# Kernel tuning notes

Hardware: AMD Instinct MI355X
Metric: run time of the kernel (lower is better)

The kernel has to match this reference:

```python
import jax, jax.numpy as jnp
import numpy as np
from jax import lax

B, C_IN, H, W = 32, 96, 48, 48
D = C_IN          # d_inner = expand(1) * in_features
K, N, DT_RANK = 2, 16, 6   # k_group, d_state, ceil(D/16)


def setup_inputs() -> dict:
    key = jax.random.key(0)
    ks = jax.random.split(key, 10)
    s = 0.02
    return {
        "x": jax.random.normal(ks[0], (B, C_IN, H, W), jnp.float32),
        "in_proj_w": jax.random.normal(ks[1], (D, C_IN)) * s,
        "in_proj_b": jnp.zeros((D,)),
        "skip_w": jax.random.normal(ks[2], (1, 1, 5)) * s,
        "skip_b": jnp.zeros((1,)),
        "conv2d_w": jax.random.normal(ks[3], (D, 1, 3, 3)) * s,
        "conv2d_b": jnp.zeros((D,)),
        "local_w": jax.random.normal(ks[4], (D, 1, 3, 3)) * s,
        "local_b": jnp.zeros((D,)),
        "bn_gamma": jnp.ones((D,)),
        "bn_beta": jnp.zeros((D,)),
        "x_proj_w": jax.random.normal(ks[5], (K, DT_RANK + 2 * N, D)) * s,
        "dt_projs_w": jax.random.normal(ks[6], (K, D, DT_RANK)) * s,
        "dt_projs_b": jax.random.normal(ks[7], (K, D)) * s,
        "A_logs": jnp.tile(jnp.log(jnp.arange(1, N + 1, dtype=jnp.float32))[None], (K * D, 1)),
        "Ds": jnp.ones((K * D,)),
        "norm_gamma": jnp.ones((D,)),
        "norm_beta": jnp.zeros((D,)),
        "out_proj_w": jax.random.normal(ks[8], (C_IN, D)) * s,
        "out_proj_b": jnp.zeros((C_IN,)),
    }


def _dwconv2d(x, w, bias):
    # depthwise 3x3, NCHW
    y = lax.conv_general_dilated(x, w, (1, 1), "SAME", feature_group_count=x.shape[1],
                                 dimension_numbers=("NCHW", "OIHW", "NCHW"))
    return y + bias[None, :, None, None]


def _forward(x, in_proj_w, in_proj_b, skip_w, skip_b, conv2d_w, conv2d_b,
             local_w, local_b, bn_gamma, bn_beta, x_proj_w, dt_projs_w,
             dt_projs_b, A_logs, Ds, norm_gamma, norm_beta, out_proj_w, out_proj_b):
    b, c, h, w = x.shape
    L = h * w
    x_in = jnp.transpose(x, (0, 2, 3, 1))                       # [B,H,W,C]
    # skip gate: Conv1d(1,1,k=5) over channel axis of the spatial mean
    zm = jnp.mean(x_in, axis=(1, 2))[:, None, :]                # [B,1,C]
    z = lax.conv_general_dilated(zm, skip_w, (1,), "SAME",
                                 dimension_numbers=("NCH", "OIH", "NCH")) + skip_b[None, :, None]
    z = z[:, None]                                              # [B,1,1,C]
    x_feat = jnp.transpose(x_in @ in_proj_w.T + in_proj_b, (0, 3, 1, 2))  # [B,D,H,W]
    x_conv = jax.nn.silu(_dwconv2d(x_feat, conv2d_w, conv2d_b))
    # ---- dynamic center-similarity ordering (computed under no_grad) ----
    xc = lax.stop_gradient(x_conv)
    xf = xc.reshape(b, D, L)
    xn = xf / jnp.maximum(jnp.linalg.norm(xf, axis=1, keepdims=True), 1e-12)
    cf = xc[:, :, h // 2, w // 2]                               # [B,D]
    cn = cf / jnp.maximum(jnp.linalg.norm(cf, axis=1, keepdims=True), 1e-12)
    sim = jnp.einsum("bdl,bd->bl", xn, cn)
    sort_idx = jnp.argsort(-sim, axis=1)                        # descending similarity
    inv_idx = jnp.argsort(sort_idx, axis=1)
    # ---- DynamicCenterScan: sorted sequence and its reverse (k_group=2) ----
    xseq = jnp.take_along_axis(x_conv.reshape(b, D, L), sort_idx[:, None, :], axis=2)
    xs = jnp.stack([xseq, jnp.flip(xseq, -1)], axis=1)          # [B,K,D,L]
    # ---- SS2D selective-scan core ----
    x_dbl = jnp.einsum("bkdl,kcd->bkcl", xs, x_proj_w)
    dts, Bs, Cs = jnp.split(x_dbl, [DT_RANK, DT_RANK + N], axis=2)
    dts = jnp.einsum("bkrl,kdr->bkdl", dts, dt_projs_w)
    dts = jax.nn.softplus(dts + dt_projs_b[None, :, :, None])   # [B,K,D,L]
    A = -jnp.exp(A_logs.reshape(K, D, N))                       # [K,D,N]

    def step(hst, t):
        dt_l, B_l, C_l, x_l = t                                 # [B,K,D],[B,K,N],[B,K,N],[B,K,D]
        dA = jnp.exp(dt_l[..., None] * A)                       # [B,K,D,N]
        hst = dA * hst + (dt_l * x_l)[..., None] * B_l[:, :, None, :]
        y = jnp.einsum("bkdn,bkn->bkd", hst, C_l)
        return hst, y

    tmove = lambda a: jnp.moveaxis(a, -1, 0)
    h0 = jnp.zeros((b, K, D, N), x.dtype)
    _, ys_t = lax.scan(step, h0, (tmove(dts), tmove(Bs), tmove(Cs), tmove(xs)))
    ys = jnp.moveaxis(ys_t, 0, -1) + Ds.reshape(K, D)[None, :, :, None] * xs  # [B,K,D,L]
    # ---- DynamicCenterMerge: un-flip, sum directions, inverse permutation ----
    y = ys[:, 0] + jnp.flip(ys[:, 1], -1)
    y = jnp.take_along_axis(y, inv_idx[:, None, :], axis=2).reshape(b, D, h, w)
    # out_norm: LayerNorm over channels
    yl = jnp.transpose(y, (0, 2, 3, 1))
    mu = jnp.mean(yl, -1, keepdims=True)
    var = jnp.var(yl, -1, keepdims=True)
    yl = (yl - mu) / jnp.sqrt(var + 1e-5) * norm_gamma + norm_beta
    out_mamba = jnp.transpose(yl, (0, 3, 1, 2))
    # local path: depthwise conv + BatchNorm (batch stats, train mode) + SiLU
    lc = _dwconv2d(x_conv, local_w, local_b)
    bm = jnp.mean(lc, (0, 2, 3))
    bv = jnp.var(lc, (0, 2, 3))
    lc = (lc - bm[None, :, None, None]) * (bn_gamma / jnp.sqrt(bv + 1e-5))[None, :, None, None] + bn_beta[None, :, None, None]
    lc = jax.nn.silu(lc)
    out = out_mamba + lc
    # softmax over dim=1 of z (singleton) == all-ones gate; kept for faithfulness
    out = jnp.transpose(out, (0, 2, 3, 1)) * jax.nn.softmax(z, axis=1)
    out = out @ out_proj_w.T + out_proj_b
    return jnp.transpose(out, (0, 3, 1, 2))


def reference(x, in_proj_w, in_proj_b, skip_w, skip_b, conv2d_w, conv2d_b,
              local_w, local_b, bn_gamma, bn_beta, x_proj_w, dt_projs_w,
              dt_projs_b, A_logs, Ds, norm_gamma, norm_beta, out_proj_w, out_proj_b):
    return _forward(x, in_proj_w, in_proj_b, skip_w, skip_b, conv2d_w, conv2d_b,
                    local_w, local_b, bn_gamma, bn_beta, x_proj_w, dt_projs_w,
                    dt_projs_b, A_logs, Ds, norm_gamma, norm_beta, out_proj_w, out_proj_b)
```

## Files before the change

kernel.cpp:

```cpp
#include <hip/hip_runtime.h>
#include <hip/hip_bf16.h>


typedef __hip_bfloat16 bf16;
__device__ __forceinline__ float b2f(bf16 v) { return __bfloat162float(v); }
__device__ __forceinline__ float ldu(const void* p, int i, bool f32) {
  if (f32) return ((const float*)p)[i];
  return b2f(((const bf16*)p)[i]);
}
__device__ __forceinline__ float rcp_f(float x) { return __builtin_amdgcn_rcpf(x); }

#define LL 2304
#define NSEG 72

#define W_INT  0
#define B_IN   9216
#define W_C2D  9312
#define B_C2D  10176
#define W_LOC  10272
#define B_LOC  11136
#define BN_G   11232
#define BN_B   11328
#define W_XPT  11424
#define W_DT   19104
#define B_DT   20256
#define A2OF   20448
#define DSOF   23520
#define LN_G   23712
#define LN_B   23808
#define W_OUTT 23904
#define B_OUT  33120
#define WBUF_N 33280ul

#define O_WBUF  0ul
#define O_XFEAT 33280ul
#define O_XCONV 7111168ul
#define O_SIM   14189056ul
#define O_SIDX  14262784ul
#define O_XST   14336512ul
#define O_XSTD  21414400ul
#define O_RBUF  28492288ul
#define O_BC    29671936ul
#define O_DSUM  34390528ul
#define O_YMLM  34832896ul
#define O_STATS 41910784ul
#define O_AFLG  41910976ul
#define O_SCSH  41911040ul
#define O_FLAG  41911232ul
#define O_END   41911296ul

__global__ void k_detect(const void* x, float* flag) {
  int i = threadIdx.x;
  bool bad = false;
  const bf16* xb = (const bf16*)x;
#pragma unroll
  for (int r = 0; r < 4; ++r) {
    float v = b2f(xb[r * 64 + i]);
    if (!(fabsf(v) <= 1e4f)) bad = true;
  }
  bool any = __any(bad);
  if (i == 0) flag[0] = any ? 1.f : 0.f;
}

__global__ void k_prep(const void* ipw, const void* ipb, const void* c2w, const void* c2b,
                       const void* lw, const void* lb, const void* bng, const void* bnb,
                       const void* xpw, const void* dtw, const void* dtb, const void* alog,
                       const void* dss, const void* ng, const void* nb, const void* opw,
                       const void* opb, float* wb, const float* flag, float* aflag) {
  bool f = flag[0] > 0.5f;
  int i = blockIdx.x * 256 + threadIdx.x;
  if (i < 9216) {
    int r = i / 96, c = i % 96;
    wb[W_INT + c * 96 + r] = ldu(ipw, i, f);
    wb[W_OUTT + c * 96 + r] = ldu(opw, i, f);
  }
  if (i < 96) {
    wb[B_IN + i] = ldu(ipb, i, f); wb[B_C2D + i] = ldu(c2b, i, f); wb[B_LOC + i] = ldu(lb, i, f);
    wb[BN_G + i] = ldu(bng, i, f); wb[BN_B + i] = ldu(bnb, i, f); wb[LN_G + i] = ldu(ng, i, f);
    wb[LN_B + i] = ldu(nb, i, f); wb[B_OUT + i] = ldu(opb, i, f);
  }
  if (i < 864) { wb[W_C2D + i] = ldu(c2w, i, f); wb[W_LOC + i] = ldu(lw, i, f); }
  if (i < 7296) {
    int k = i / 3648, c = (i / 96) % 38, d = i % 96;
    wb[W_XPT + d * 80 + k * 38 + c] = ldu(xpw, i, f);
  }
  if (i < 1152) wb[W_DT + i] = ldu(dtw, i, f);
  if (i < 192) { wb[B_DT + i] = ldu(dtb, i, f); wb[DSOF + i] = ldu(dss, i, f); }
  if (i < 3072) {
    float av = expf(ldu(alog, i, f));
    wb[A2OF + i] = -av * 1.4426950408889634f;
    int n = i % 16;
    if (fabsf(av - (float)(n + 1)) > 1e-3f * (n + 1)) atomicAdd(aflag, 1.f);
  }
}

__global__ __launch_bounds__(128, 4)
void k_inproj(const void* __restrict__ x, const float* __restrict__ wb,
              float* __restrict__ xfeat, const float* __restrict__ flag) {
  int b = blockIdx.x / 36;
  int rest = blockIdx.x % 36;
  int half = rest / 18;
  int l = (rest % 18) * 128 + threadIdx.x;
  float acc[48];
#pragma unroll
  for (int j = 0; j < 48; ++j) acc[j] = wb[B_IN + half * 48 + j];
  bool f = flag[0] > 0.5f;
  if (f) {
    const float* xf = (const float*)x;
#pragma unroll 2
    for (int c = 0; c < 96; ++c) {
      float xc = xf[(b * 96 + c) * LL + l];
      const float* wr = wb + W_INT + c * 96 + half * 48;
#pragma unroll
      for (int j = 0; j < 48; ++j) acc[j] += xc * wr[j];
    }
  } else {
    const bf16* xb = (const bf16*)x;
#pragma unroll 2
    for (int c = 0; c < 96; ++c) {
      float xc = b2f(xb[(b * 96 + c) * LL + l]);
      const float* wr = wb + W_INT + c * 96 + half * 48;
#pragma unroll
      for (int j = 0; j < 48; ++j) acc[j] += xc * wr[j];
    }
  }
#pragma unroll
  for (int j = 0; j < 48; ++j) xfeat[(b * 96 + half * 48 + j) * LL + l] = acc[j];
}

__global__ __launch_bounds__(256, 8)
void k_conv_silu(const float* __restrict__ xfeat, const float* __restrict__ wb,
                 float* __restrict__ xconv) {
  int t = blockIdx.x * 256 + threadIdx.x;
  int l = t % LL; int d = (t / LL) % 96; int b = t / (LL * 96);
  int h = l / 48, w = l % 48;
  const float* wr = wb + W_C2D + d * 9;
  const float* src = xfeat + (b * 96 + d) * LL;
  float acc = wb[B_C2D + d];
#pragma unroll
  for (int ki = 0; ki < 3; ++ki) {
    int hh = h + ki - 1; if (hh < 0 || hh >= 48) continue;
#pragma unroll
    for (int kj = 0; kj < 3; ++kj) {
      int ww = w + kj - 1; if (ww < 0 || ww >= 48) continue;
      acc += src[hh * 48 + ww] * wr[ki * 3 + kj];
    }
  }
  xconv[t] = acc / (1.f + expf(-acc));
}

__global__ __launch_bounds__(256, 8)
void k_sim(const float* __restrict__ xconv, float* __restrict__ sim) {
  int b = blockIdx.x / 9;
  int l = (blockIdx.x % 9) * 256 + threadIdx.x;
  const float* base = xconv + (size_t)b * 96 * LL;
  float dot = 0, nrm = 0, cn = 0;
  for (int d = 0; d < 96; ++d) {
    float v = base[d * LL + l];
    float c = base[d * LL + 1176];
    dot += v * c; nrm += v * v; cn += c * c;
  }
  float den = fmaxf(sqrtf(nrm), 1e-12f) * fmaxf(sqrtf(cn), 1e-12f);
  sim[b * LL + l] = dot / den;
}

__global__ void k_sort(const float* __restrict__ sim, int* __restrict__ sidx) {
  __shared__ unsigned long long key[4096];
  int b = blockIdx.x;
  for (int i = threadIdx.x; i < 4096; i += 1024) {
    unsigned long long kv = ~0ull;
    if (i < LL) {
      unsigned u = __float_as_uint(sim[b * LL + i]);
      u = (u >> 31) ? ~u : (u | 0x80000000u);
      kv = (((unsigned long long)(~u)) << 32) | (unsigned)i;
    }
    key[i] = kv;
  }
  __syncthreads();
  for (int k = 2; k <= 4096; k <<= 1)
    for (int j = k >> 1; j > 0; j >>= 1) {
      for (int i = threadIdx.x; i < 4096; i += 1024) {
        int ij = i ^ j;
        if (ij > i) {
          unsigned long long a = key[i], c = key[ij];
          bool up = ((i & k) == 0);
          if ((a > c) == up) { key[i] = c; key[ij] = a; }
        }
      }
      __syncthreads();
    }
  for (int i = threadIdx.x; i < LL; i += 1024) sidx[b * LL + i] = (int)(key[i] & 0xffffffffu);
}

__global__ __launch_bounds__(256, 8)
void k_gatherd(const float* __restrict__ xconv, const int* __restrict__ sidx,
               float* __restrict__ xstd) {
  int t = blockIdx.x * 256 + threadIdx.x;
  int l = t % LL; int d = (t / LL) % 96; int b = t / (LL * 96);
  int p = sidx[b * LL + l];
  xstd[t] = xconv[((size_t)b * 96 + d) * LL + p];
}

__global__ __launch_bounds__(256, 4)
void k_tr_dl(const float* __restrict__ in, float* __restrict__ out) {
  __shared__ float tile[64 * 97];
  int b = blockIdx.x / 36;
  int l0 = (blockIdx.x % 36) * 64;
#pragma unroll
  for (int it = 0; it < 24; ++it) {
    int idx = it * 256 + threadIdx.x;
    int d = idx / 64, j = idx % 64;
    tile[j * 97 + d] = in[((size_t)b * 96 + d) * LL + l0 + j];
  }
  __syncthreads();
#pragma unroll
  for (int it = 0; it < 24; ++it) {
    int idx = it * 256 + threadIdx.x;
    int r = idx / 96, c = idx % 96;
    out[((size_t)b * LL + l0 + r) * 96 + c] = tile[r * 97 + c];
  }
}

__global__ __launch_bounds__(256, 4)
void k_tr_ld(const float* __restrict__ in, float* __restrict__ out) {
  __shared__ float tile[64 * 97];
  int b = blockIdx.x / 36;
  int l0 = (blockIdx.x % 36) * 64;
#pragma unroll
  for (int it = 0; it < 24; ++it) {
    int idx = it * 256 + threadIdx.x;
    int r = idx / 96, c = idx % 96;
    tile[r * 97 + c] = in[((size_t)b * LL + l0 + r) * 96 + c];
  }
  __syncthreads();
#pragma unroll
  for (int it = 0; it < 24; ++it) {
    int idx = it * 256 + threadIdx.x;
    int d = idx / 64, j = idx % 64;
    out[((size_t)b * 96 + d) * LL + l0 + j] = tile[j * 97 + d];
  }
}

template <int KSEL>
__global__ __launch_bounds__(128, 4)
void k_xdbl(const float* __restrict__ xstd, const float* __restrict__ wb,
            float* __restrict__ rbuf, float* __restrict__ bc) {
  int b = blockIdx.x / 18;
  int l = (blockIdx.x % 18) * 128 + threadIdx.x;
  float acc[38];
#pragma unroll
  for (int j = 0; j < 38; ++j) acc[j] = 0.f;
#pragma unroll 2
  for (int c = 0; c < 96; ++c) {
    float xc = xstd[((size_t)b * 96 + c) * LL + l];
    const float* wr = wb + W_XPT + c * 80 + KSEL * 38;
#pragma unroll
    for (int j = 0; j < 38; ++j) acc[j] += xc * wr[j];
  }
  int lout = KSEL ? (LL - 1 - l) : l;
  float4* r4 = (float4*)(rbuf + ((size_t)(b * 2 + KSEL) * LL + lout) * 8);
  r4[0] = make_float4(acc[0], acc[1], acc[2], acc[3]);
  r4[1] = make_float4(acc[4], acc[5], 0.f, 0.f);
  float4* b4 = (float4*)(bc + ((size_t)(b * 2 + KSEL) * LL + lout) * 32);
#pragma unroll
  for (int i = 0; i < 8; ++i)
    b4[i] = make_float4(acc[6 + 4 * i], acc[7 + 4 * i], acc[8 + 4 * i], acc[9 + 4 * i]);
}

__global__ __launch_bounds__(192, 4)
void k_scan1(const float* __restrict__ rbuf, const float* __restrict__ bc,
             const float* __restrict__ xst, const float* __restrict__ wb,
             float* __restrict__ dsum, float* __restrict__ hend,
             const float* __restrict__ aflag) {
  __shared__ float sbc[2][1024];
  __shared__ float srr[2][256];
  int sub = threadIdx.x / 96;
  int tid = threadIdx.x - sub * 96;
  int unit = blockIdx.x * 2 + sub;
  int s = unit % 72; int k = (unit / 72) % 2; int b = unit / 144;
  int lbase = (b * 2 + k) * LL + s * 32;
  {
    const float4* bsrc = (const float4*)(bc + (size_t)lbase * 32);
    float4* bdst = (float4*)sbc[sub];
    for (int i = tid; i < 256; i += 96) bdst[i] = bsrc[i];
    const float4* rsrc = (const float4*)(rbuf + (size_t)lbase * 8);
    float4* rdst = (float4*)srr[sub];
    if (tid < 64) rdst[tid] = rsrc[tid];
  }
  __syncthreads();
  int d = tid;
  float wd[6];
#pragma unroll
  for (int j = 0; j < 6; ++j) wd[j] = wb[W_DT + (k * 96 + d) * 6 + j];
  float bd = wb[B_DT + k * 96 + d];
  float h[16];
#pragma unroll
  for (int n = 0; n < 16; ++n) h[n] = 0.f;
  float ds = 0.f;
  long long lk0 = k ? (LL - 1 - s * 32) : (s * 32);
  long long stp = k ? -96 : 96;
  const float* xp = xst + (size_t)b * LL * 96 + lk0 * 96 + d;
  bool fast = (aflag[0] == 0.f);
  if (fast) {
#pragma unroll 4
    for (int t = 0; t < 32; ++t) {
      float xv = *xp; xp += stp;
      const float* rr = &srr[sub][t * 8];
      float a = bd + rr[0] * wd[0] + rr[1] * wd[1] + rr[2] * wd[2]
                   + rr[3] * wd[3] + rr[4] * wd[4] + rr[5] * wd[5];
      float ea = __expf(a);
      float p1 = rcp_f(1.f + ea);
      float dtv = (a > 20.f) ? a : -0.69314718055994531f * __log2f(p1);
      ds += dtv;
      float dtx = dtv * xv;
      const float* bcl = &sbc[sub][t * 32];
      float p2 = p1 * p1, p3 = p2 * p1, p4 = p2 * p2, p5 = p4 * p1, p6 = p4 * p2,
            p7 = p4 * p3, p8 = p4 * p4, p9 = p8 * p1, p10 = p8 * p2, p11 = p8 * p3,
            p12 = p8 * p4, p13 = p8 * p5, p14 = p8 * p6, p15 = p8 * p7, p16 = p8 * p8;
      h[0] = p1 * h[0] + dtx * bcl[0];   h[1] = p2 * h[1] + dtx * bcl[1];
      h[2] = p3 * h[2] + dtx * bcl[2];   h[3] = p4 * h[3] + dtx * bcl[3];
      h[4] = p5 * h[4] + dtx * bcl[4];   h[5] = p6 * h[5] + dtx * bcl[5];
      h[6] = p7 * h[6] + dtx * bcl[6];   h[7] = p8 * h[7] + dtx * bcl[7];
      h[8] = p9 * h[8] + dtx * bcl[8];   h[9] = p10 * h[9] + dtx * bcl[9];
      h[10] = p11 * h[10] + dtx * bcl[10]; h[11] = p12 * h[11] + dtx * bcl[11];
      h[12] = p13 * h[12] + dtx * bcl[12]; h[13] = p14 * h[13] + dtx * bcl[13];
      h[14] = p15 * h[14] + dtx * bcl[14]; h[15] = p16 * h[15] + dtx * bcl[15];
    }
  } else {
    float a2[16];
#pragma unroll
    for (int n = 0; n < 16; ++n) a2[n] = wb[A2OF + (k * 96 + d) * 16 + n];
#pragma unroll 4
    for (int t = 0; t < 32; ++t) {
      float xv = *xp; xp += stp;
      const float* rr = &srr[sub][t * 8];
      float a = bd + rr[0] * wd[0] + rr[1] * wd[1] + rr[2] * wd[2]
                   + rr[3] * wd[3] + rr[4] * wd[4] + rr[5] * wd[5];
      float dtv = (a > 20.f) ? a : log1pf(expf(a));
      ds += dtv;
      float dtx = dtv * xv;
      const float* bcl = &sbc[sub][t * 32];
#pragma unroll
      for (int n = 0; n < 16; ++n) h[n] = exp2f(dtv * a2[n]) * h[n] + dtx * bcl[n];
    }
  }
  dsum[((b * 2 + k) * 96 + d) * NSEG + s] = ds;
  float4* ho = (float4*)(hend + (((size_t)(b * 2 + k) * NSEG + s) * 96 + d) * 16);
  ho[0] = make_float4(h[0], h[1], h[2], h[3]);
  ho[1] = make_float4(h[4], h[5], h[6], h[7]);
  ho[2] = make_float4(h[8], h[9], h[10], h[11]);
  ho[3] = make_float4(h[12], h[13], h[14], h[15]);
}

__global__ __launch_bounds__(256, 4)
void k_scan2(const float* __restrict__ dsum, const float* __restrict__ hend,
             const float* __restrict__ wb, float* __restrict__ hstart) {
  int t = blockIdx.x * 256 + threadIdx.x;
  int n = t % 16; int d = (t / 16) % 96; int k = (t / 1536) % 2; int b = t / 3072;
  float a2 = wb[A2OF + (k * 96 + d) * 16 + n];
  float h = 0.f;
  int rowd = ((b * 2 + k) * 96 + d) * NSEG;
  for (int s = 0; s < NSEG; ++s) {
    size_t idx = (((size_t)(b * 2 + k) * NSEG + s) * 96 + d) * 16 + n;
    hstart[idx] = h;
    h = exp2f(a2 * dsum[rowd + s]) * h + hend[idx];
  }
}

__global__ __launch_bounds__(192, 4)
void k_scan3ln(const float* __restrict__ rbuf, const float* __restrict__ bc,
               const float* __restrict__ xst, const float* __restrict__ wb,
               const float* __restrict__ hstart, const int* __restrict__ sidx,
               float* __restrict__ ymlm, const float* __restrict__ aflag) {
  __shared__ float yA[32 * 97];
  __shared__ float yB[32 * 97];
  __shared__ float sbc[2][1024];
  __shared__ float srr[2][256];
  __shared__ float smu[32], srs[32];
  int b = blockIdx.x / NSEG;
  int u = blockIdx.x % NSEG;
  int t = threadIdx.x;
  int sub = t / 96;
  int d = t - sub * 96;
  int k = sub;
  int seg = sub ? (NSEG - 1 - u) : u;
  int lbase = (b * 2 + k) * LL + seg * 32;
  {
    const float4* bsrc = (const float4*)(bc + (size_t)lbase * 32);
    float4* bdst = (float4*)sbc[sub];
    for (int i = d; i < 256; i += 96) bdst[i] = bsrc[i];
    const float4* rsrc = (const float4*)(rbuf + (size_t)lbase * 8);
    float4* rdst = (float4*)srr[sub];
    if (d < 64) rdst[d] = rsrc[d];
  }
  __syncthreads();
  {
    float* yacc = sub ? yB : yA;
    float wd[6];
#pragma unroll
    for (int j = 0; j < 6; ++j) wd[j] = wb[W_DT + (k * 96 + d) * 6 + j];
    float bd = wb[B_DT + k * 96 + d];
    float Dv = wb[DSOF + k * 96 + d];
    float h[16];
    const float* hi = hstart + (((size_t)(b * 2 + k) * NSEG + seg) * 96 + d) * 16;
#pragma unroll
    for (int n = 0; n < 16; ++n) h[n] = hi[n];
    long long lk0 = k ? (LL - 1 - seg * 32) : (seg * 32);
    long long stp = k ? -96 : 96;
    const float* xp = xst + (size_t)b * LL * 96 + lk0 * 96 + d;
    bool fast = (aflag[0] == 0.f);
    if (fast) {
#pragma unroll 4
      for (int i = 0; i < 32; ++i) {
        float xv = *xp; xp += stp;
        const float* rr = &srr[sub][i * 8];
        float a = bd + rr[0] * wd[0] + rr[1] * wd[1] + rr[2] * wd[2]
                     + rr[3] * wd[3] + rr[4] * wd[4] + rr[5] * wd[5];
        float ea = __expf(a);
        float p1 = rcp_f(1.f + ea);
        float dtv = (a > 20.f) ? a : -0.69314718055994531f * __log2f(p1);
        float dtx = dtv * xv;
        const float* bcl = &sbc[sub][i * 32];
        float p2 = p1 * p1, p3 = p2 * p1, p4 = p2 * p2, p5 = p4 * p1, p6 = p4 * p2,
              p7 = p4 * p3, p8 = p4 * p4, p9 = p8 * p1, p10 = p8 * p2, p11 = p8 * p3,
              p12 = p8 * p4, p13 = p8 * p5, p14 = p8 * p6, p15 = p8 * p7, p16 = p8 * p8;
        float y;
        h[0] = p1 * h[0] + dtx * bcl[0];   y  = h[0] * bcl[16];
        h[1] = p2 * h[1] + dtx * bcl[1];   y += h[1] * bcl[17];
        h[2] = p3 * h[2] + dtx * bcl[2];   y += h[2] * bcl[18];
        h[3] = p4 * h[3] + dtx * bcl[3];   y += h[3] * bcl[19];
        h[4] = p5 * h[4] + dtx * bcl[4];   y += h[4] * bcl[20];
        h[5] = p6 * h[5] + dtx * bcl[5];   y += h[5] * bcl[21];
        h[6] = p7 * h[6] + dtx * bcl[6];   y += h[6] * bcl[22];
        h[7] = p8 * h[7] + dtx * bcl[7];   y += h[7] * bcl[23];
        h[8] = p9 * h[8] + dtx * bcl[8];   y += h[8] * bcl[24];
        h[9] = p10 * h[9] + dtx * bcl[9];  y += h[9] * bcl[25];
        h[10] = p11 * h[10] + dtx * bcl[10]; y += h[10] * bcl[26];
        h[11] = p12 * h[11] + dtx * bcl[11]; y += h[11] * bcl[27];
        h[12] = p13 * h[12] + dtx * bcl[12]; y += h[12] * bcl[28];
        h[13] = p14 * h[13] + dtx * bcl[13]; y += h[13] * bcl[29];
        h[14] = p15 * h[14] + dtx * bcl[14]; y += h[14] * bcl[30];
        h[15] = p16 * h[15] + dtx * bcl[15]; y += h[15] * bcl[31];
        int qloc = k ? (31 - i) : i;
        yacc[qloc * 97 + d] = y + Dv * xv;
      }
    } else {
      float a2[16];
#pragma unroll
      for (int n = 0; n < 16; ++n) a2[n] = wb[A2OF + (k * 96 + d) * 16 + n];
#pragma unroll 4
      for (int i = 0; i < 32; ++i) {
        float xv = *xp; xp += stp;
        const float* rr = &srr[sub][i * 8];
        float a = bd + rr[0] * wd[0] + rr[1] * wd[1] + rr[2] * wd[2]
                     + rr[3] * wd[3] + rr[4] * wd[4] + rr[5] * wd[5];
        float dtv = (a > 20.f) ? a : log1pf(expf(a));
        float dtx = dtv * xv;
        const float* bcl = &sbc[sub][i * 32];
        float y = 0.f;
#pragma unroll
        for (int n = 0; n < 16; ++n) {
          h[n] = exp2f(dtv * a2[n]) * h[n] + dtx * bcl[n];
          y += h[n] * bcl[16 + n];
        }
        int qloc = k ? (31 - i) : i;
        yacc[qloc * 97 + d] = y + Dv * xv;
      }
    }
  }
  __syncthreads();
  if (t < 32) {
    float sum = 0, ss = 0;
#pragma unroll
    for (int dd = 0; dd < 96; ++dd) {
      float v = yA[t * 97 + dd] + yB[t * 97 + dd];
      sum += v; ss += v * v;
    }
    float mu = sum * (1.f / 96.f);
    float var = ss * (1.f / 96.f) - mu * mu;
    smu[t] = mu;
    srs[t] = rsqrtf(var + 1e-5f);
  }
  __syncthreads();
  {
    int r = t / 6, c0 = (t % 6) * 16;
    int q = u * 32 + r;
    int p = sidx[b * LL + q];
    float mu = smu[r], rs = srs[r];
    float tmp[16];
#pragma unroll
    for (int j = 0; j < 16; ++j) {
      int dd = c0 + j;
      tmp[j] = (yA[r * 97 + dd] + yB[r * 97 + dd] - mu) * rs * wb[LN_G + dd] + wb[LN_B + dd];
    }
    float4* o4 = (float4*)(ymlm + ((size_t)b * LL + p) * 96 + c0);
    o4[0] = make_float4(tmp[0], tmp[1], tmp[2], tmp[3]);
    o4[1] = make_float4(tmp[4], tmp[5], tmp[6], tmp[7]);
    o4[2] = make_float4(tmp[8], tmp[9], tmp[10], tmp[11]);
    o4[3] = make_float4(tmp[12], tmp[13], tmp[14], tmp[15]);
  }
}

__global__ __launch_bounds__(256, 8)
void k_convlc_bn(const float* __restrict__ xconv, const float* __restrict__ wb,
                 float* __restrict__ lcbuf, float* __restrict__ stats) {
  int bd = blockIdx.x;
  int b = bd / 96, d = bd % 96;
  const float* src = xconv + (size_t)(b * 96 + d) * LL;
  const float* wr = wb + W_LOC + d * 9;
  float bias = wb[B_LOC + d];
  float s1 = 0, s2 = 0;
  for (int l = threadIdx.x; l < LL; l += 256) {
    int h = l / 48, w = l % 48;
    float acc = bias;
#pragma unroll
    for (int ki = 0; ki < 3; ++ki) {
      int hh = h + ki - 1; if (hh < 0 || hh >= 48) continue;
#pragma unroll
      for (int kj = 0; kj < 3; ++kj) {
        int ww = w + kj - 1; if (ww < 0 || ww >= 48) continue;
        acc += src[hh * 48 + ww] * wr[ki * 3 + kj];
      }
    }
    lcbuf[(size_t)(b * 96 + d) * LL + l] = acc;
    s1 += acc; s2 += acc * acc;
  }
  __shared__ float r1[256], r2[256];
  r1[threadIdx.x] = s1; r2[threadIdx.x] = s2; __syncthreads();
  for (int o = 128; o > 0; o >>= 1) {
    if (threadIdx.x < o) { r1[threadIdx.x] += r1[threadIdx.x + o]; r2[threadIdx.x] += r2[threadIdx.x + o]; }
    __syncthreads();
  }
  if (threadIdx.x == 0) { atomicAdd(&stats[d], r1[0]); atomicAdd(&stats[96 + d], r2[0]); }
}

__global__ void k_bnfin(const float* __restrict__ stats, const float* __restrict__ wb,
                        float* __restrict__ scsh) {
  int d = threadIdx.x; if (d >= 96) return;
  float mean = stats[d] * (1.f / 73728.f);
  float var = stats[96 + d] * (1.f / 73728.f) - mean * mean;
  float sc = wb[BN_G + d] * rsqrtf(var + 1e-5f);
  scsh[d] = sc; scsh[96 + d] = wb[BN_B + d] - mean * sc;
}

__global__ __launch_bounds__(128, 4)
void k_final(const float* __restrict__ lcbuf, const float* __restrict__ ymdm,
             const float* __restrict__ wb, const float* __restrict__ scsh,
             void* __restrict__ out, const float* __restrict__ flag) {
  int b = blockIdx.x / 36;
  int rest = blockIdx.x % 36;
  int half = rest / 18;
  int l = (rest % 18) * 128 + threadIdx.x;
  float acc[48];
#pragma unroll
  for (int j = 0; j < 48; ++j) acc[j] = wb[B_OUT + half * 48 + j];
#pragma unroll 2
  for (int d = 0; d < 96; ++d) {
    float lc = lcbuf[((size_t)b * 96 + d) * LL + l] * scsh[d] + scsh[96 + d];
    float vd = lc * rcp_f(1.f + __expf(-lc)) + ymdm[((size_t)b * 96 + d) * LL + l];
    const float* wr = wb + W_OUTT + d * 96 + half * 48;
#pragma unroll
    for (int j = 0; j < 48; ++j) acc[j] += vd * wr[j];
  }
  bool f = flag[0] > 0.5f;
  if (f) {
    float* of = (float*)out;
#pragma unroll
    for (int j = 0; j < 48; ++j) of[(b * 96 + half * 48 + j) * LL + l] = acc[j];
  } else {
    bf16* ob = (bf16*)out;
#pragma unroll
    for (int j = 0; j < 48; ++j) ob[(b * 96 + half * 48 + j) * LL + l] = __float2bfloat16(acc[j]);
  }
}

extern "C" void kernel_launch(void* const* d_in, const int* in_sizes, int n_in,
                              void* d_out, int out_size, void* d_ws, size_t ws_size,
                              hipStream_t stream) {
  if (ws_size < O_END * sizeof(float)) return;
  float* ws = (float*)d_ws;
  float* wb    = ws + O_WBUF;
  float* xfeat = ws + O_XFEAT;
  float* xconv = ws + O_XCONV;
  float* sim   = ws + O_SIM;
  int*   sidx  = (int*)(ws + O_SIDX);
  float* xst   = ws + O_XST;
  float* xstd  = ws + O_XSTD;
  float* rbuf  = ws + O_RBUF;
  float* bc    = ws + O_BC;
  float* dsum  = ws + O_DSUM;
  float* ymlm  = ws + O_YMLM;
  float* stats = ws + O_STATS;
  float* aflag = ws + O_AFLG;
  float* scsh  = ws + O_SCSH;
  float* flag  = ws + O_FLAG;
  float* hend   = xfeat;
  float* hstart = xstd;
  float* ymdm   = xfeat;
  float* lcbuf  = xst;

  hipMemsetAsync(stats, 0, 256 * sizeof(float), stream);
  k_detect<<<1, 64, 0, stream>>>(d_in[0], flag);
  k_prep<<<36, 256, 0, stream>>>(
      d_in[1], d_in[2], d_in[5], d_in[6], d_in[7], d_in[8], d_in[9], d_in[10],
      d_in[11], d_in[12], d_in[13], d_in[14], d_in[15], d_in[16], d_in[17], d_in[18],
      d_in[19], wb, flag, aflag);
  k_inproj<<<1152, 128, 0, stream>>>(d_in[0], wb, xfeat, flag);
  k_conv_silu<<<27648, 256, 0, stream>>>(xfeat, wb, xconv);
  k_sim<<<288, 256, 0, stream>>>(xconv, sim);
  k_sort<<<32, 1024, 0, stream>>>(sim, sidx);
  k_gatherd<<<27648, 256, 0, stream>>>(xconv, sidx, xstd);
  k_tr_dl<<<1152, 256, 0, stream>>>(xstd, xst);
  k_xdbl<0><<<576, 128, 0, stream>>>(xstd, wb, rbuf, bc);
  k_xdbl<1><<<576, 128, 0, stream>>>(xstd, wb, rbuf, bc);
  k_scan1<<<2304, 192, 0, stream>>>(rbuf, bc, xst, wb, dsum, hend, aflag);
  k_scan2<<<384, 256, 0, stream>>>(dsum, hend, wb, hstart);
  k_scan3ln<<<2304, 192, 0, stream>>>(rbuf, bc, xst, wb, hstart, sidx, ymlm, aflag);
  k_tr_ld<<<1152, 256, 0, stream>>>(ymlm, ymdm);
  k_convlc_bn<<<3072, 256, 0, stream>>>(xconv, wb, lcbuf, stats);
  k_bnfin<<<1, 96, 0, stream>>>(stats, wb, scsh);
  k_final<<<1152, 128, 0, stream>>>(lcbuf, ymdm, wb, scsh, d_out, flag);
}
```

Before: 576.3 us.

## Vectorize selective scan with packed float2 math and prefetch x into registers

Rewrites the fast path of the two chunked-scan kernels to update state pairs with 2-wide float vectors, so the compiler can emit packed FMA instructions, and reads B/C and dt rows from shared memory as float4. All 32 x values per segment are loaded into registers before the shared-memory staging, overlapping global latency with the cooperative copy, and the inner loop is fully unrolled. Occupancy bounds are lowered from 4 to 3 blocks to leave room for the extra registers, and the inter-segment scan loop gets an unroll 8 hint. The risk is reduced occupancy and register pressure from the 32-entry prefetch array.

```diff
diff --git a/kernel.cpp b/kernel.cpp
--- a/kernel.cpp
+++ b/kernel.cpp
@@ -3,6 +3,10 @@
 
 
 typedef __hip_bfloat16 bf16;
+typedef float v2f __attribute__((ext_vector_type(2)));
+typedef float v4f __attribute__((ext_vector_type(4)));
+#define SH2(V, a, b) __builtin_shufflevector(V, V, a, b)
+
 __device__ __forceinline__ float b2f(bf16 v) { return __bfloat162float(v); }
 __device__ __forceinline__ float ldu(const void* p, int i, bool f32) {
   if (f32) return ((const float*)p)[i];
@@ -267,7 +271,7 @@
     b4[i] = make_float4(acc[6 + 4 * i], acc[7 + 4 * i], acc[8 + 4 * i], acc[9 + 4 * i]);
 }
 
-__global__ __launch_bounds__(192, 4)
+__global__ __launch_bounds__(192, 3)
 void k_scan1(const float* __restrict__ rbuf, const float* __restrict__ bc,
              const float* __restrict__ xst, const float* __restrict__ wb,
              float* __restrict__ dsum, float* __restrict__ hend,
@@ -279,6 +283,12 @@
   int unit = blockIdx.x * 2 + sub;
   int s = unit % 72; int k = (unit / 72) % 2; int b = unit / 144;
   int lbase = (b * 2 + k) * LL + s * 32;
+  long long lk0 = k ? (LL - 1 - s * 32) : (s * 32);
+  long long stp = k ? -96 : 96;
+  const float* xp = xst + (size_t)b * LL * 96 + lk0 * 96 + tid;
+  float xv[32];
+#pragma unroll
+  for (int t = 0; t < 32; ++t) xv[t] = xp[t * stp];
   {
     const float4* bsrc = (const float4*)(bc + (size_t)lbase * 32);
     float4* bdst = (float4*)sbc[sub];
@@ -293,63 +303,72 @@
 #pragma unroll
   for (int j = 0; j < 6; ++j) wd[j] = wb[W_DT + (k * 96 + d) * 6 + j];
   float bd = wb[B_DT + k * 96 + d];
-  float h[16];
-#pragma unroll
-  for (int n = 0; n < 16; ++n) h[n] = 0.f;
   float ds = 0.f;
-  long long lk0 = k ? (LL - 1 - s * 32) : (s * 32);
-  long long stp = k ? -96 : 96;
-  const float* xp = xst + (size_t)b * LL * 96 + lk0 * 96 + d;
+  v2f h2[8];
+#pragma unroll
+  for (int j = 0; j < 8; ++j) h2[j] = (v2f){0.f, 0.f};
   bool fast = (aflag[0] == 0.f);
   if (fast) {
-#pragma unroll 4
+    const v4f* bq4 = (const v4f*)sbc[sub];
+    const v4f* rq4 = (const v4f*)srr[sub];
+#pragma unroll
     for (int t = 0; t < 32; ++t) {
-      float xv = *xp; xp += stp;
-      const float* rr = &srr[sub][t * 8];
-      float a = bd + rr[0] * wd[0] + rr[1] * wd[1] + rr[2] * wd[2]
-                   + rr[3] * wd[3] + rr[4] * wd[4] + rr[5] * wd[5];
+      v4f r0 = rq4[t * 2], r1 = rq4[t * 2 + 1];
+      float a = bd + r0.x * wd[0] + r0.y * wd[1] + r0.z * wd[2]
+                   + r0.w * wd[3] + r1.x * wd[4] + r1.y * wd[5];
       float ea = __expf(a);
       float p1 = rcp_f(1.f + ea);
       float dtv = (a > 20.f) ? a : -0.69314718055994531f * __log2f(p1);
       ds += dtv;
-      float dtx = dtv * xv;
-      const float* bcl = &sbc[sub][t * 32];
-      float p2 = p1 * p1, p3 = p2 * p1, p4 = p2 * p2, p5 = p4 * p1, p6 = p4 * p2,
-            p7 = p4 * p3, p8 = p4 * p4, p9 = p8 * p1, p10 = p8 * p2, p11 = p8 * p3,
-            p12 = p8 * p4, p13 = p8 * p5, p14 = p8 * p6, p15 = p8 * p7, p16 = p8 * p8;
-      h[0] = p1 * h[0] + dtx * bcl[0];   h[1] = p2 * h[1] + dtx * bcl[1];
-      h[2] = p3 * h[2] + dtx * bcl[2];   h[3] = p4 * h[3] + dtx * bcl[3];
-      h[4] = p5 * h[4] + dtx * bcl[4];   h[5] = p6 * h[5] + dtx * bcl[5];
-      h[6] = p7 * h[6] + dtx * bcl[6];   h[7] = p8 * h[7] + dtx * bcl[7];
-      h[8] = p9 * h[8] + dtx * bcl[8];   h[9] = p10 * h[9] + dtx * bcl[9];
-      h[10] = p11 * h[10] + dtx * bcl[10]; h[11] = p12 * h[11] + dtx * bcl[11];
-      h[12] = p13 * h[12] + dtx * bcl[12]; h[13] = p14 * h[13] + dtx * bcl[13];
-      h[14] = p15 * h[14] + dtx * bcl[14]; h[15] = p16 * h[15] + dtx * bcl[15];
+      float dtx = dtv * xv[t];
+      v2f dt2 = {dtx, dtx};
+      float p2s = p1 * p1;
+      v2f P1 = {p1, p2s};
+      v2f P2 = P1 * (v2f){p2s, p2s};
+      float p4s = P2.y;
+      v2f P3 = P1 * (v2f){p4s, p4s};
+      v2f P4 = P2 * (v2f){p4s, p4s};
+      float p8s = P4.y;
+      v2f P5 = P1 * (v2f){p8s, p8s};
+      v2f P6 = P2 * (v2f){p8s, p8s};
+      v2f P7 = P3 * (v2f){p8s, p8s};
+      v2f P8 = P4 * (v2f){p8s, p8s};
+      v4f B0 = bq4[t * 8 + 0], B1 = bq4[t * 8 + 1];
+      v4f B2 = bq4[t * 8 + 2], B3 = bq4[t * 8 + 3];
+      h2[0] = P1 * h2[0] + dt2 * SH2(B0, 0, 1);
+      h2[1] = P2 * h2[1] + dt2 * SH2(B0, 2, 3);
+      h2[2] = P3 * h2[2] + dt2 * SH2(B1, 0, 1);
+      h2[3] = P4 * h2[3] + dt2 * SH2(B1, 2, 3);
+      h2[4] = P5 * h2[4] + dt2 * SH2(B2, 0, 1);
+      h2[5] = P6 * h2[5] + dt2 * SH2(B2, 2, 3);
+      h2[6] = P7 * h2[6] + dt2 * SH2(B3, 0, 1);
+      h2[7] = P8 * h2[7] + dt2 * SH2(B3, 2, 3);
     }
   } else {
-    float a2[16];
-#pragma unroll
-    for (int n = 0; n < 16; ++n) a2[n] = wb[A2OF + (k * 96 + d) * 16 + n];
+    float a2[16], hh[16];
+#pragma unroll
+    for (int n = 0; n < 16; ++n) { a2[n] = wb[A2OF + (k * 96 + d) * 16 + n]; hh[n] = 0.f; }
 #pragma unroll 4
     for (int t = 0; t < 32; ++t) {
-      float xv = *xp; xp += stp;
       const float* rr = &srr[sub][t * 8];
       float a = bd + rr[0] * wd[0] + rr[1] * wd[1] + rr[2] * wd[2]
                    + rr[3] * wd[3] + rr[4] * wd[4] + rr[5] * wd[5];
       float dtv = (a > 20.f) ? a : log1pf(expf(a));
       ds += dtv;
-      float dtx = dtv * xv;
+      float dtx = dtv * xv[t];
       const float* bcl = &sbc[sub][t * 32];
 #pragma unroll
-      for (int n = 0; n < 16; ++n) h[n] = exp2f(dtv * a2[n]) * h[n] + dtx * bcl[n];
-    }
+      for (int n = 0; n < 16; ++n) hh[n] = exp2f(dtv * a2[n]) * hh[n] + dtx * bcl[n];
+    }
+#pragma unroll
+    for (int j = 0; j < 8; ++j) h2[j] = (v2f){hh[2 * j], hh[2 * j + 1]};
   }
   dsum[((b * 2 + k) * 96 + d) * NSEG + s] = ds;
   float4* ho = (float4*)(hend + (((size_t)(b * 2 + k) * NSEG + s) * 96 + d) * 16);
-  ho[0] = make_float4(h[0], h[1], h[2], h[3]);
-  ho[1] = make_float4(h[4], h[5], h[6], h[7]);
-  ho[2] = make_float4(h[8], h[9], h[10], h[11]);
-  ho[3] = make_float4(h[12], h[13], h[14], h[15]);
+  ho[0] = make_float4(h2[0].x, h2[0].y, h2[1].x, h2[1].y);
+  ho[1] = make_float4(h2[2].x, h2[2].y, h2[3].x, h2[3].y);
+  ho[2] = make_float4(h2[4].x, h2[4].y, h2[5].x, h2[5].y);
+  ho[3] = make_float4(h2[6].x, h2[6].y, h2[7].x, h2[7].y);
 }
 
 __global__ __launch_bounds__(256, 4)
@@ -360,6 +379,7 @@
   float a2 = wb[A2OF + (k * 96 + d) * 16 + n];
   float h = 0.f;
   int rowd = ((b * 2 + k) * 96 + d) * NSEG;
+#pragma unroll 8
   for (int s = 0; s < NSEG; ++s) {
     size_t idx = (((size_t)(b * 2 + k) * NSEG + s) * 96 + d) * 16 + n;
     hstart[idx] = h;
@@ -367,7 +387,7 @@
   }
 }
 
-__global__ __launch_bounds__(192, 4)
+__global__ __launch_bounds__(192, 3)
 void k_scan3ln(const float* __restrict__ rbuf, const float* __restrict__ bc,
                const float* __restrict__ xst, const float* __restrict__ wb,
                const float* __restrict__ hstart, const int* __restrict__ sidx,
@@ -385,6 +405,12 @@
   int k = sub;
   int seg = sub ? (NSEG - 1 - u) : u;
   int lbase = (b * 2 + k) * LL + seg * 32;
+  long long lk0 = k ? (LL - 1 - seg * 32) : (seg * 32);
+  long long stp = k ? -96 : 96;
+  const float* xp = xst + (size_t)b * LL * 96 + lk0 * 96 + d;
+  float xv[32];
+#pragma unroll
+  for (int i = 0; i < 32; ++i) xv[i] = xp[i * stp];
   {
     const float4* bsrc = (const float4*)(bc + (size_t)lbase * 32);
     float4* bdst = (float4*)sbc[sub];
@@ -401,70 +427,75 @@
     for (int j = 0; j < 6; ++j) wd[j] = wb[W_DT + (k * 96 + d) * 6 + j];
     float bd = wb[B_DT + k * 96 + d];
     float Dv = wb[DSOF + k * 96 + d];
-    float h[16];
     const float* hi = hstart + (((size_t)(b * 2 + k) * NSEG + seg) * 96 + d) * 16;
-#pragma unroll
-    for (int n = 0; n < 16; ++n) h[n] = hi[n];
-    long long lk0 = k ? (LL - 1 - seg * 32) : (seg * 32);
-    long long stp = k ? -96 : 96;
-    const float* xp = xst + (size_t)b * LL * 96 + lk0 * 96 + d;
     bool fast = (aflag[0] == 0.f);
     if (fast) {
-#pragma unroll 4
+      const v4f* hi4 = (const v4f*)hi;
+      v4f H0 = hi4[0], H1 = hi4[1], H2 = hi4[2], H3 = hi4[3];
+      v2f h2[8];
+      h2[0] = SH2(H0, 0, 1); h2[1] = SH2(H0, 2, 3);
+      h2[2] = SH2(H1, 0, 1); h2[3] = SH2(H1, 2, 3);
+      h2[4] = SH2(H2, 0, 1); h2[5] = SH2(H2, 2, 3);
+      h2[6] = SH2(H3, 0, 1); h2[7] = SH2(H3, 2, 3);
+      const v4f* bq4 = (const v4f*)sbc[sub];
+      const v4f* rq4 = (const v4f*)srr[sub];
+#pragma unroll
       for (int i = 0; i < 32; ++i) {
-        float xv = *xp; xp += stp;
-        const float* rr = &srr[sub][i * 8];
-        float a = bd + rr[0] * wd[0] + rr[1] * wd[1] + rr[2] * wd[2]
-                     + rr[3] * wd[3] + rr[4] * wd[4] + rr[5] * wd[5];
+        v4f r0 = rq4[i * 2], r1 = rq4[i * 2 + 1];
+        float a = bd + r0.x * wd[0] + r0.y * wd[1] + r0.z * wd[2]
+                     + r0.w * wd[3] + r1.x * wd[4] + r1.y * wd[5];
         float ea = __expf(a);
         float p1 = rcp_f(1.f + ea);
         float dtv = (a > 20.f) ? a : -0.69314718055994531f * __log2f(p1);
-        float dtx = dtv * xv;
-        const float* bcl = &sbc[sub][i * 32];
-        float p2 = p1 * p1, p3 = p2 * p1, p4 = p2 * p2, p5 = p4 * p1, p6 = p4 * p2,
-              p7 = p4 * p3, p8 = p4 * p4, p9 = p8 * p1, p10 = p8 * p2, p11 = p8 * p3,
-              p12 = p8 * p4, p13 = p8 * p5, p14 = p8 * p6, p15 = p8 * p7, p16 = p8 * p8;
-        float y;
-        h[0] = p1 * h[0] + dtx * bcl[0];   y  = h[0] * bcl[16];
-        h[1] = p2 * h[1] + dtx * bcl[1];   y += h[1] * bcl[17];
-        h[2] = p3 * h[2] + dtx * bcl[2];   y += h[2] * bcl[18];
-        h[3] = p4 * h[3] + dtx * bcl[3];   y += h[3] * bcl[19];
-        h[4] = p5 * h[4] + dtx * bcl[4];   y += h[4] * bcl[20];
-        h[5] = p6 * h[5] + dtx * bcl[5];   y += h[5] * bcl[21];
-        h[6] = p7 * h[6] + dtx * bcl[6];   y += h[6] * bcl[22];
-        h[7] = p8 * h[7] + dtx * bcl[7];   y += h[7] * bcl[23];
-        h[8] = p9 * h[8] + dtx * bcl[8];   y += h[8] * bcl[24];
-        h[9] = p10 * h[9] + dtx * bcl[9];  y += h[9] * bcl[25];
-        h[10] = p11 * h[10] + dtx * bcl[10]; y += h[10] * bcl[26];
-        h[11] = p12 * h[11] + dtx * bcl[11]; y += h[11] * bcl[27];
-        h[12] = p13 * h[12] + dtx * bcl[12]; y += h[12] * bcl[28];
-        h[13] = p14 * h[13] + dtx * bcl[13]; y += h[13] * bcl[29];
-        h[14] = p15 * h[14] + dtx * bcl[14]; y += h[14] * bcl[30];
-        h[15] = p16 * h[15] + dtx * bcl[15]; y += h[15] * bcl[31];
+        float dtx = dtv * xv[i];
+        v2f dt2 = {dtx, dtx};
+        float p2s = p1 * p1;
+        v2f P1 = {p1, p2s};
+        v2f P2 = P1 * (v2f){p2s, p2s};
+        float p4s = P2.y;
+        v2f P3 = P1 * (v2f){p4s, p4s};
+        v2f P4 = P2 * (v2f){p4s, p4s};
+        float p8s = P4.y;
+        v2f P5 = P1 * (v2f){p8s, p8s};
+        v2f P6 = P2 * (v2f){p8s, p8s};
+        v2f P7 = P3 * (v2f){p8s, p8s};
+        v2f P8 = P4 * (v2f){p8s, p8s};
+        v4f B0 = bq4[i * 8 + 0], B1 = bq4[i * 8 + 1];
+        v4f B2 = bq4[i * 8 + 2], B3 = bq4[i * 8 + 3];
+        v4f C0 = bq4[i * 8 + 4], C1 = bq4[i * 8 + 5];
+        v4f C2 = bq4[i * 8 + 6], C3 = bq4[i * 8 + 7];
+        v2f y2;
+        h2[0] = P1 * h2[0] + dt2 * SH2(B0, 0, 1); y2  = h2[0] * SH2(C0, 0, 1);
+        h2[1] = P2 * h2[1] + dt2 * SH2(B0, 2, 3); y2 += h2[1] * SH2(C0, 2, 3);
+        h2[2] = P3 * h2[2] + dt2 * SH2(B1, 0, 1); y2 += h2[2] * SH2(C1, 0, 1);
+        h2[3] = P4 * h2[3] + dt2 * SH2(B1, 2, 3); y2 += h2[3] * SH2(C1, 2, 3);
+        h2[4] = P5 * h2[4] + dt2 * SH2(B2, 0, 1); y2 += h2[4] * SH2(C2, 0, 1);
+        h2[5] = P6 * h2[5] + dt2 * SH2(B2, 2, 3); y2 += h2[5] * SH2(C2, 2, 3);
+        h2[6] = P7 * h2[6] + dt2 * SH2(B3, 0, 1); y2 += h2[6] * SH2(C3, 0, 1);
+        h2[7] = P8 * h2[7] + dt2 * SH2(B3, 2, 3); y2 += h2[7] * SH2(C3, 2, 3);
         int qloc = k ? (31 - i) : i;
-        yacc[qloc * 97 + d] = y + Dv * xv;
+        yacc[qloc * 97 + d] = y2.x + y2.y + Dv * xv[i];
       }
     } else {
-      float a2[16];
-#pragma unroll
-      for (int n = 0; n < 16; ++n) a2[n] = wb[A2OF + (k * 96 + d) * 16 + n];
+      float a2[16], hh[16];
+#pragma unroll
+      for (int n = 0; n < 16; ++n) { a2[n] = wb[A2OF + (k * 96 + d) * 16 + n]; hh[n] = hi[n]; }
 #pragma unroll 4
       for (int i = 0; i < 32; ++i) {
-        float xv = *xp; xp += stp;
         const float* rr = &srr[sub][i * 8];
         float a = bd + rr[0] * wd[0] + rr[1] * wd[1] + rr[2] * wd[2]
                      + rr[3] * wd[3] + rr[4] * wd[4] + rr[5] * wd[5];
         float dtv = (a > 20.f) ? a : log1pf(expf(a));
-        float dtx = dtv * xv;
+        float dtx = dtv * xv[i];
         const float* bcl = &sbc[sub][i * 32];
         float y = 0.f;
 #pragma unroll
         for (int n = 0; n < 16; ++n) {
-          h[n] = exp2f(dtv * a2[n]) * h[n] + dtx * bcl[n];
-          y += h[n] * bcl[16 + n];
+          hh[n] = exp2f(dtv * a2[n]) * hh[n] + dtx * bcl[n];
+          y += hh[n] * bcl[16 + n];
         }
         int qloc = k ? (31 - i) : i;
-        yacc[qloc * 97 + d] = y + Dv * xv;
+        yacc[qloc * 97 + d] = y + Dv * xv[i];
       }
     }
   }
```

Result: no change. 565.1 us (-1.9%).
